# Kernel optimization log

Hardware: AMD Instinct MI355X
Metric: run time of the kernel (lower is better)

## Reference

```python
import jax, jax.numpy as jnp
import numpy as np

RANK = 3
NUM_STEPS = 3
NUM_ENT = 40000
NUM_EMB = 24
NUM_OPS = 12
DIM = 128
HID = 128
BATCH = 128
NNZ = 300000


def _lstm_dir(x, Wih, Whh, bih, bhh, reverse=False):
    # x: (S, B, D); PyTorch gate order i, f, g, o
    B = x.shape[1]
    H = Whh.shape[1]
    def step(carry, xt):
        h, c = carry
        z = xt @ Wih.T + h @ Whh.T + bih + bhh  # (B, 4H)
        i, f, g, o = jnp.split(z, 4, axis=-1)
        c = jax.nn.sigmoid(f) * c + jax.nn.sigmoid(i) * jnp.tanh(g)
        h = jax.nn.sigmoid(o) * jnp.tanh(c)
        return (h, c), h
    init = (jnp.zeros((B, H), x.dtype), jnp.zeros((B, H), x.dtype))
    _, hs = jax.lax.scan(step, init, x, reverse=reverse)
    return hs  # (S, B, H)


def _spmm(memory, src, dst, val, num_ent):
    # memory: (B, E); edges (src -> dst): out[b, j] = sum_{e: dst[e]=j} memory[b, src[e]] * val[e]
    g = memory[:, src] * val[None, :]              # (B, nnz)
    out = jax.ops.segment_sum(g.T, dst, num_segments=num_ent)  # (E, B)
    return out.T


def setup_inputs() -> dict:
    key = jax.random.key(0)
    ks = jax.random.split(key, 16)
    inp = {
        'queries': jax.random.randint(ks[0], (BATCH,), 0, NUM_EMB),
        'heads': jax.random.randint(ks[1], (BATCH,), 0, NUM_ENT),
        'edge_src': jax.random.randint(ks[2], (NUM_OPS, NNZ), 0, NUM_ENT, dtype=jnp.int32),
        'edge_dst': jax.random.randint(ks[3], (NUM_OPS, NNZ), 0, NUM_ENT, dtype=jnp.int32),
        'edge_val': jax.random.uniform(ks[4], (NUM_OPS, NNZ), jnp.float32),
        'emb': jax.random.normal(ks[5], (NUM_EMB, DIM), jnp.float32) * 0.1,
        'Wih_f': jax.random.normal(ks[6], (RANK, 4 * HID, DIM), jnp.float32) * 0.1,
        'Whh_f': jax.random.normal(ks[7], (RANK, 4 * HID, HID), jnp.float32) * 0.1,
        'bih_f': jnp.zeros((RANK, 4 * HID), jnp.float32),
        'bhh_f': jnp.zeros((RANK, 4 * HID), jnp.float32),
        'Wih_b': jax.random.normal(ks[8], (RANK, 4 * HID, DIM), jnp.float32) * 0.1,
        'Whh_b': jax.random.normal(ks[9], (RANK, 4 * HID, HID), jnp.float32) * 0.1,
        'bih_b': jnp.zeros((RANK, 4 * HID), jnp.float32),
        'bhh_b': jnp.zeros((RANK, 4 * HID), jnp.float32),
        'W0': jax.random.normal(ks[10], (2 * HID, NUM_OPS + 1), jnp.float32) * 0.1,
        'b0': jnp.zeros((1, NUM_OPS + 1), jnp.float32),
    }
    return inp


def reference(queries, heads, edge_src, edge_dst, edge_val, emb,
              Wih_f, Whh_f, bih_f, bhh_f, Wih_b, Whh_b, bih_b, bhh_b, W0, b0):
    # query embedding replicated over time: (S, B, D)
    q = emb[queries]
    x = jnp.broadcast_to(q[None], (NUM_STEPS, q.shape[0], q.shape[1]))
    head_onehot = jax.nn.one_hot(heads, NUM_ENT, dtype=jnp.float32)  # (B, E)

    logits = jnp.zeros((q.shape[0], NUM_ENT), jnp.float32)
    for r in range(RANK):
        hf = _lstm_dir(x, Wih_f[r], Whh_f[r], bih_f[r], bhh_f[r], reverse=False)
        hb = _lstm_dir(x, Wih_b[r], Whh_b[r], bih_b[r], bhh_b[r], reverse=True)
        rnn_out = jnp.concatenate([hf, hb], axis=-1)          # (S, B, 2H)
        trans = rnn_out @ W0 + b0                             # (S, B, ops+1)
        attn = jax.nn.softmax(trans, axis=-1)
        attn = jnp.transpose(attn, (0, 2, 1))                 # (S, ops+1, B)

        memory = head_onehot                                  # (B, E)
        for t in range(NUM_STEPS):
            attn_t = attn[t]                                  # (ops+1, B)
            acc = memory * attn_t[-1][:, None]                # identity operator
            for op in range(NUM_OPS):
                prod = _spmm(memory, edge_src[op], edge_dst[op], edge_val[op], NUM_ENT)
                acc = acc + prod * attn_t[op][:, None]
            memory = acc
        norm = jnp.maximum(jnp.float32(1e-20), jnp.sum(memory, axis=1, keepdims=True))
        logits = logits + memory / norm
    return logits
```

## Files before the change

kernel.cpp:

```cpp
#include <hip/hip_runtime.h>

#define NENT 40000
#define NB 128
#define NQ 24
#define NOPS 12
#define EPO 300000
#define NTOT (NOPS * EPO)
#define NRANK 3
#define NPASS 8
#define CP 16
#define ECAP 160

typedef float v4f __attribute__((ext_vector_type(4)));

__device__ __forceinline__ v4f shfl_xor4(v4f x, int m) {
    v4f r;
    r.x = __shfl_xor(x.x, m);
    r.y = __shfl_xor(x.y, m);
    r.z = __shfl_xor(x.z, m);
    r.w = __shfl_xor(x.w, m);
    return r;
}

__device__ __forceinline__ bool bittest(const unsigned* bm, int i) {
    return (bm[i >> 5] >> (i & 31)) & 1u;
}

__global__ void headmark_kernel(const int* __restrict__ heads, unsigned* __restrict__ bmH,
                                unsigned* __restrict__ bm2) {
    int h = heads[threadIdx.x];
    atomicOr(&bmH[h >> 5], 1u << (h & 31));
    atomicOr(&bm2[h >> 5], 1u << (h & 31));
}

__global__ void mark2_kernel(const int* __restrict__ src, const int* __restrict__ dst,
                             const unsigned* __restrict__ bmH, unsigned* __restrict__ bm2) {
    int i = blockIdx.x * 256 + threadIdx.x;
    if (i < NTOT) {
        int s = src[i];
        if (bittest(bmH, s)) {
            int d = dst[i];
            atomicOr(&bm2[d >> 5], 1u << (d & 31));
        }
    }
}

__global__ void build_ell_kernel(const int* __restrict__ src, const int* __restrict__ dst,
                                 const float* __restrict__ val, const unsigned* __restrict__ bm2,
                                 int* __restrict__ fillD, int* __restrict__ fillS,
                                 int2* __restrict__ eD, int2* __restrict__ eS) {
    int i = blockIdx.x * 256 + threadIdx.x;
    if (i >= NTOT) return;
    int s = src[i], d = dst[i];
    int op = i / EPO;
    int v = __float_as_int(val[i]);
    int pd = atomicAdd(&fillD[d], 1);
    eD[(size_t)d * ECAP + pd] = make_int2(s | (op << 16), v);
    if (bittest(bm2, s)) {
        int ps = atomicAdd(&fillS[s], 1);
        eS[(size_t)s * ECAP + ps] = make_int2(d | (op << 16), v);
    }
}

__global__ void zxq_kernel(const float* __restrict__ emb,
                           const float* __restrict__ Wih_f, const float* __restrict__ bih_f,
                           const float* __restrict__ bhh_f,
                           const float* __restrict__ Wih_b, const float* __restrict__ bih_b,
                           const float* __restrict__ bhh_b,
                           float* __restrict__ zxq) {
    int combo = blockIdx.x / NQ;
    int q = blockIdx.x % NQ;
    int dir = combo / 3, r = combo % 3;
    const float* Wih = (dir ? Wih_b : Wih_f) + r * 512 * 128;
    const float* bih = (dir ? bih_b : bih_f) + r * 512;
    const float* bhh = (dir ? bhh_b : bhh_f) + r * 512;
    __shared__ float x[128];
    int u = threadIdx.x;
    x[u] = emb[q * 128 + u];
    __syncthreads();
    const float* W0p = Wih + u * 128;
    const float* W1p = Wih + (128 + u) * 128;
    const float* W2p = Wih + (256 + u) * 128;
    const float* W3p = Wih + (384 + u) * 128;
    float a0 = 0.f, a1 = 0.f, a2 = 0.f, a3 = 0.f;
    for (int d = 0; d < 128; ++d) {
        float xv = x[d];
        a0 = fmaf(xv, W0p[d], a0);
        a1 = fmaf(xv, W1p[d], a1);
        a2 = fmaf(xv, W2p[d], a2);
        a3 = fmaf(xv, W3p[d], a3);
    }
    float* o = zxq + (size_t)(combo * NQ + q) * 512;
    o[u]       = a0 + bih[u]       + bhh[u];
    o[128 + u] = a1 + bih[128 + u] + bhh[128 + u];
    o[256 + u] = a2 + bih[256 + u] + bhh[256 + u];
    o[384 + u] = a3 + bih[384 + u] + bhh[384 + u];
}

__global__ void lstmq_kernel(const float* __restrict__ Whh_f, const float* __restrict__ Whh_b,
                             const float* __restrict__ zxq, float* __restrict__ hq) {
    int combo = blockIdx.x / NQ;
    int q = blockIdx.x % NQ;
    int dir = combo / 3, r = combo % 3;
    const float* Whh = (dir ? Whh_b : Whh_f) + r * 512 * 128;
    __shared__ float h[128];
    int u = threadIdx.x;
    const float* z = zxq + (size_t)(combo * NQ + q) * 512;
    float zi0 = z[u], zf0 = z[128 + u], zg0 = z[256 + u], zo0 = z[384 + u];
    const float* Wi = Whh + u * 128;
    const float* Wf = Whh + (128 + u) * 128;
    const float* Wg = Whh + (256 + u) * 128;
    const float* Wo = Whh + (384 + u) * 128;
    float c = 0.f;
    h[u] = 0.f;
    for (int s = 0; s < 3; ++s) {
        __syncthreads();
        float a0 = 0.f, a1 = 0.f, a2 = 0.f, a3 = 0.f;
        for (int d = 0; d < 128; ++d) {
            float hv = h[d];
            a0 = fmaf(hv, Wi[d], a0);
            a1 = fmaf(hv, Wf[d], a1);
            a2 = fmaf(hv, Wg[d], a2);
            a3 = fmaf(hv, Wo[d], a3);
        }
        float ig = 1.f / (1.f + expf(-(zi0 + a0)));
        float fg = 1.f / (1.f + expf(-(zf0 + a1)));
        float gg = tanhf(zg0 + a2);
        float og = 1.f / (1.f + expf(-(zo0 + a3)));
        c = fg * c + ig * gg;
        float hn = og * tanhf(c);
        __syncthreads();
        h[u] = hn;
        hq[(size_t)((combo * 3 + s) * NQ + q) * 128 + u] = hn;
    }
}

__global__ void attnq_kernel(const float* __restrict__ hq, const float* __restrict__ W0,
                             const float* __restrict__ b0, float* __restrict__ attnq) {
    int r = blockIdx.x / 3, t = blockIdx.x % 3;
    __shared__ float W0s[256 * 13];
    for (int idx = threadIdx.x; idx < 256 * 13; idx += 32) W0s[idx] = W0[idx];
    __syncthreads();
    int q = threadIdx.x;
    if (q >= NQ) return;
    float acc[13];
    for (int k = 0; k < 13; ++k) acc[k] = b0[k];
    const float* hf = hq + (size_t)(((0 * 3 + r) * 3 + t) * NQ + q) * 128;
    const float* hb = hq + (size_t)(((1 * 3 + r) * 3 + (2 - t)) * NQ + q) * 128;
    for (int u = 0; u < 128; ++u) {
        float v = hf[u];
        for (int k = 0; k < 13; ++k) acc[k] = fmaf(v, W0s[u * 13 + k], acc[k]);
    }
    for (int u = 0; u < 128; ++u) {
        float v = hb[u];
        for (int k = 0; k < 13; ++k) acc[k] = fmaf(v, W0s[(128 + u) * 13 + k], acc[k]);
    }
    float m = acc[0];
    for (int k = 1; k < 13; ++k) m = fmaxf(m, acc[k]);
    float e[13];
    float sum = 0.f;
    for (int k = 0; k < 13; ++k) { e[k] = expf(acc[k] - m); sum += e[k]; }
    float inv = 1.f / sum;
    float* ao = attnq + (size_t)(r * 3 + t) * 13 * NQ;
    for (int k = 0; k < 13; ++k) ao[k * NQ + q] = e[k] * inv;
}

__global__ void expand_kernel(const int* __restrict__ queries, const float* __restrict__ attnq,
                              float* __restrict__ attn) {
    __shared__ int qs[128];
    if (threadIdx.x < 128) qs[threadIdx.x] = queries[threadIdx.x];
    __syncthreads();
    for (int idx = threadIdx.x; idx < 9 * 13 * 128; idx += 256) {
        int b = idx & 127, kk = idx >> 7;
        attn[idx] = attnq[kk * NQ + qs[b]];
    }
}

__global__ void fused01_kernel(const int* __restrict__ heads, const float* __restrict__ attn,
                               const int* __restrict__ fillS, const int2* __restrict__ eS,
                               float* __restrict__ mem2) {
    int r = blockIdx.y;
    int b = blockIdx.x;
    int chunk = blockIdx.z;
    __shared__ float c0s[13], c1s[13];
    if (threadIdx.x < 13) {
        c0s[threadIdx.x] = attn[(size_t)((r * 3 + 0) * 13 + threadIdx.x) * 128 + b];
        c1s[threadIdx.x] = attn[(size_t)((r * 3 + 1) * 13 + threadIdx.x) * 128 + b];
    }
    __syncthreads();
    int h = heads[b];
    int lenH = fillS[h];
    float* mem = mem2 + ((size_t)(r * NPASS + (b >> 4)) * NENT) * CP + (b & 15);
    int g = threadIdx.x >> 3, lane8 = threadIdx.x & 7;
    for (int ent = g + chunk * 32; ent < lenH + 1; ent += 64) {
        int i; float wv;
        if (ent == 0) { i = h; wv = c0s[12]; }
        else {
            int2 e = eS[(size_t)h * ECAP + ent - 1];
            i = e.x & 0xFFFF;
            wv = __int_as_float(e.y) * c0s[e.x >> 16];
        }
        if (lane8 == 0) atomicAdd(&mem[(size_t)i * CP], c1s[12] * wv);
        int lenI = fillS[i];
        const int2* ei = eS + (size_t)i * ECAP;
        for (int f = lane8; f < lenI; f += 8) {
            int2 e2 = ei[f];
            atomicAdd(&mem[(size_t)(e2.x & 0xFFFF) * CP],
                      __int_as_float(e2.y) * c1s[e2.x >> 16] * wv);
        }
    }
}

struct EStage { int2 a, b, c, d; };
struct GStage { v4f a, b, c, d; };

#define ISSUE_E(E, bb) { int bi = (bb) + slot; \
    E.a = edp0[bi < l0 ? bi : 0]; \
    E.b = edp1[bi < l1 ? bi : 0]; \
    E.c = edp2[bi < l2 ? bi : 0]; \
    E.d = edp3[bi < l3 ? bi : 0]; }

#define ISSUE_G(G, E) { \
    G.a = *(const v4f*)(inr + (size_t)(E.a.x & 0xFFFF) * CP + cq4); \
    G.b = *(const v4f*)(inr + (size_t)(E.b.x & 0xFFFF) * CP + cq4); \
    G.c = *(const v4f*)(inr + (size_t)(E.c.x & 0xFFFF) * CP + cq4); \
    G.d = *(const v4f*)(inr + (size_t)(E.d.x & 0xFFFF) * CP + cq4); }

#define CONSUME_P(G, E, bb) { int bi = (bb) + slot; \
    { v4f cc = *(const v4f*)&cs[(E.a.x >> 16) * 20 + cq4]; \
      float w = bi < l0 ? __int_as_float(E.a.y) : 0.f; acc0 += (w * cc) * G.a; } \
    { v4f cc = *(const v4f*)&cs[(E.b.x >> 16) * 20 + cq4]; \
      float w = bi < l1 ? __int_as_float(E.b.y) : 0.f; acc1 += (w * cc) * G.b; } \
    { v4f cc = *(const v4f*)&cs[(E.c.x >> 16) * 20 + cq4]; \
      float w = bi < l2 ? __int_as_float(E.c.y) : 0.f; acc2 += (w * cc) * G.c; } \
    { v4f cc = *(const v4f*)&cs[(E.d.x >> 16) * 20 + cq4]; \
      float w = bi < l3 ? __int_as_float(E.d.y) : 0.f; acc3 += (w * cc) * G.d; } }

#define REDUCE_ROW(A, T) { \
    v4f red = A; \
    red += shfl_xor4(red, 4); \
    red += shfl_xor4(red, 8); \
    red += shfl_xor4(red, 16); \
    red += shfl_xor4(red, 32); \
    if (slot == 0) { \
        int j = jw + (T); \
        v4f mi = *(const v4f*)(inr + (size_t)j * CP + cq4); \
        v4f res = cid * mi + red; \
        *(v4f*)(outr + (size_t)j * CP + cq4) = res; \
        rsum += res; \
    } }

__global__ __launch_bounds__(256) void dense_kernel(const float* __restrict__ attn,
                                                    const int* __restrict__ fillD,
                                                    const int2* __restrict__ edgesD,
                                                    const float* __restrict__ in,
                                                    float* __restrict__ out,
                                                    float* __restrict__ normv) {
    int p = blockIdx.x;
    int r = blockIdx.z;
    __shared__ __align__(16) float cs[13 * 20];
    __shared__ float npart[4][16];
    int tid = threadIdx.x;
    if (tid < 13 * 16) {
        int op = tid >> 4, c0 = tid & 15;
        cs[op * 20 + c0] = attn[(size_t)((r * 3 + 2) * 13 + op) * 128 + p * CP + c0];
    }
    __syncthreads();
    int wave = tid >> 6, lane = tid & 63;
    int slot = lane >> 2;
    int cq4 = (lane & 3) * 4;
    int jw = blockIdx.y * 16 + wave * 4;
    const float* inr = in + (size_t)(r * NPASS + p) * NENT * CP;
    float* outr = out + (size_t)(r * NPASS + p) * NENT * CP;
    int l0 = fillD[jw], l1 = fillD[jw + 1], l2 = fillD[jw + 2], l3 = fillD[jw + 3];
    const int2* edp0 = edgesD + (size_t)(jw + 0) * ECAP;
    const int2* edp1 = edgesD + (size_t)(jw + 1) * ECAP;
    const int2* edp2 = edgesD + (size_t)(jw + 2) * ECAP;
    const int2* edp3 = edgesD + (size_t)(jw + 3) * ECAP;
    int maxlen = max(max(l0, l1), max(l2, l3));
    v4f acc0 = (v4f)0.f, acc1 = (v4f)0.f, acc2 = (v4f)0.f, acc3 = (v4f)0.f;

    EStage E0, E1, E2;
    GStage G0, G1, G2;
    ISSUE_E(E0, 0)
    ISSUE_E(E1, 16)
    ISSUE_E(E2, 32)
    ISSUE_G(G0, E0)
    ISSUE_G(G1, E1)
    int nb = (maxlen + 15) >> 4;
    int R = (nb + 2) / 3;
    int base = 0;
    for (int rr = 0; rr < R; ++rr, base += 48) {
        CONSUME_P(G0, E0, base)
        ISSUE_E(E0, base + 48)
        ISSUE_G(G2, E2)
        CONSUME_P(G1, E1, base + 16)
        ISSUE_E(E1, base + 64)
        ISSUE_G(G0, E0)
        CONSUME_P(G2, E2, base + 32)
        ISSUE_E(E2, base + 80)
        ISSUE_G(G1, E1)
    }

    v4f cid = *(const v4f*)&cs[12 * 20 + cq4];
    v4f rsum = (v4f)0.f;
    REDUCE_ROW(acc0, 0)
    REDUCE_ROW(acc1, 1)
    REDUCE_ROW(acc2, 2)
    REDUCE_ROW(acc3, 3)
    if (slot == 0) *(v4f*)&npart[wave][cq4] = rsum;
    __syncthreads();
    if (tid < 16) {
        float s = npart[0][tid] + npart[1][tid] + npart[2][tid] + npart[3][tid];
        atomicAdd(&normv[r * 128 + p * CP + tid], s);
    }
}

__global__ void rnorm_kernel(const float* __restrict__ normv, float* __restrict__ rnormv) {
    int i = threadIdx.x;
    rnormv[i] = 1.f / fmaxf(normv[i], 1e-20f);
}

__global__ void final_kernel(const float* __restrict__ mem3, const float* __restrict__ rnormv,
                             float* __restrict__ out) {
    __shared__ float tile[32 * 129];
    __shared__ float rn[384];
    for (int idx = threadIdx.x; idx < 384; idx += 256) rn[idx] = rnormv[idx];
    __syncthreads();
    int j0 = blockIdx.x * 32;
    for (int p = 0; p < NPASS; ++p) {
        for (int it = 0; it < 2; ++it) {
            int lin = it * 256 + threadIdx.x;
            int jj = lin >> 4, c = lin & 15;
            int b = p * CP + c;
            float s = 0.f;
            for (int r = 0; r < 3; ++r)
                s += mem3[((size_t)(r * NPASS + p) * NENT + j0 + jj) * CP + c] * rn[r * 128 + b];
            tile[jj * 129 + b] = s;
        }
    }
    __syncthreads();
    for (int it = 0; it < 16; ++it) {
        int lin = it * 256 + threadIdx.x;
        int b = lin >> 5, jj = lin & 31;
        out[(size_t)b * NENT + j0 + jj] = tile[jj * 129 + b];
    }
}

extern "C" void kernel_launch(void* const* d_in, const int* in_sizes, int n_in,
                              void* d_out, int out_size, void* d_ws, size_t ws_size,
                              hipStream_t stream) {
    const int*   queries  = (const int*)d_in[0];
    const int*   heads    = (const int*)d_in[1];
    const int*   edge_src = (const int*)d_in[2];
    const int*   edge_dst = (const int*)d_in[3];
    const float* edge_val = (const float*)d_in[4];
    const float* emb      = (const float*)d_in[5];
    const float* Wih_f    = (const float*)d_in[6];
    const float* Whh_f    = (const float*)d_in[7];
    const float* bih_f    = (const float*)d_in[8];
    const float* bhh_f    = (const float*)d_in[9];
    const float* Wih_b    = (const float*)d_in[10];
    const float* Whh_b    = (const float*)d_in[11];
    const float* bih_b    = (const float*)d_in[12];
    const float* bhh_b    = (const float*)d_in[13];
    const float* W0       = (const float*)d_in[14];
    const float* b0       = (const float*)d_in[15];
    float* out = (float*)d_out;

    char* w = (char*)d_ws;
    size_t off = 0;
    auto alloc = [&](size_t bytes) -> void* {
        off = (off + 255) & ~(size_t)255;
        void* p = w + off;
        off += bytes;
        return p;
    };
    float* attnq  = (float*)alloc((size_t)9 * 13 * NQ * sizeof(float));
    float* attn   = (float*)alloc((size_t)9 * 13 * 128 * sizeof(float));
    float* zxq    = (float*)alloc((size_t)6 * NQ * 512 * sizeof(float));
    float* hq     = (float*)alloc((size_t)6 * 3 * NQ * 128 * sizeof(float));
    unsigned* bmH = (unsigned*)alloc((2 * 1250 + 2 * NENT) * sizeof(int));
    unsigned* bm2 = bmH + 1250;
    int* fillD    = (int*)(bm2 + 1250);
    int* fillS    = fillD + NENT;
    int2*  eD     = (int2*)alloc((size_t)NENT * ECAP * sizeof(int2));
    float* mem2   = (float*)alloc((size_t)NRANK * NENT * NB * sizeof(float));
    float* mem3   = (float*)alloc((size_t)NRANK * NENT * NB * sizeof(float));
    int2*  eS     = (int2*)mem3;
    float* normv  = (float*)alloc((size_t)NRANK * NB * sizeof(float));
    float* rnormv = (float*)alloc((size_t)NRANK * NB * sizeof(float));

    int cooGrid = (NTOT + 255) / 256;

    hipMemsetAsync(bmH, 0, (2 * 1250 + 2 * NENT) * sizeof(int), stream);
    headmark_kernel<<<1, 128, 0, stream>>>(heads, bmH, bm2);
    mark2_kernel<<<cooGrid, 256, 0, stream>>>(edge_src, edge_dst, bmH, bm2);
    build_ell_kernel<<<cooGrid, 256, 0, stream>>>(edge_src, edge_dst, edge_val, bm2,
                                                  fillD, fillS, eD, eS);

    zxq_kernel<<<6 * NQ, 128, 0, stream>>>(emb, Wih_f, bih_f, bhh_f, Wih_b, bih_b, bhh_b, zxq);
    lstmq_kernel<<<6 * NQ, 128, 0, stream>>>(Whh_f, Whh_b, zxq, hq);
    attnq_kernel<<<9, 32, 0, stream>>>(hq, W0, b0, attnq);
    expand_kernel<<<1, 256, 0, stream>>>(queries, attnq, attn);

    hipMemsetAsync(mem2, 0, (size_t)NRANK * NENT * NB * sizeof(float), stream);
    hipMemsetAsync(normv, 0, NRANK * NB * sizeof(float), stream);
    {
        dim3 g(NB, NRANK, 2);
        fused01_kernel<<<g, 256, 0, stream>>>(heads, attn, fillS, eS, mem2);
    }
    {
        dim3 g(NPASS, NENT / 16, NRANK);
        dense_kernel<<<g, 256, 0, stream>>>(attn, fillD, eD, mem2, mem3, normv);
    }

    rnorm_kernel<<<1, NRANK * NB, 0, stream>>>(normv, rnormv);
    final_kernel<<<NENT / 32, 256, 0, stream>>>(mem3, rnormv, out);
}
```

Before: 1.271 ms.

## Process all three ranks per dense block to share edge loads

The dense SpMM kernel now handles all three ranks in a single block instead of one rank per grid z-slice. Each ELL edge entry is loaded once and reused for three gathers, which cuts edge-list traffic and index decoding by a factor of three. The hand-written three-stage software pipeline of edge and gather loads is replaced by a simple loop. This trades the explicit latency hiding and some occupancy (twelve accumulators, a third as many blocks) for fewer redundant edge loads.

```diff
diff --git a/kernel.cpp b/kernel.cpp
--- a/kernel.cpp
+++ b/kernel.cpp
@@ -211,32 +211,19 @@
     }
 }
 
-struct EStage { int2 a, b, c, d; };
-struct GStage { v4f a, b, c, d; };
-
-#define ISSUE_E(E, bb) { int bi = (bb) + slot; \
-    E.a = edp0[bi < l0 ? bi : 0]; \
-    E.b = edp1[bi < l1 ? bi : 0]; \
-    E.c = edp2[bi < l2 ? bi : 0]; \
-    E.d = edp3[bi < l3 ? bi : 0]; }
-
-#define ISSUE_G(G, E) { \
-    G.a = *(const v4f*)(inr + (size_t)(E.a.x & 0xFFFF) * CP + cq4); \
-    G.b = *(const v4f*)(inr + (size_t)(E.b.x & 0xFFFF) * CP + cq4); \
-    G.c = *(const v4f*)(inr + (size_t)(E.c.x & 0xFFFF) * CP + cq4); \
-    G.d = *(const v4f*)(inr + (size_t)(E.d.x & 0xFFFF) * CP + cq4); }
-
-#define CONSUME_P(G, E, bb) { int bi = (bb) + slot; \
-    { v4f cc = *(const v4f*)&cs[(E.a.x >> 16) * 20 + cq4]; \
-      float w = bi < l0 ? __int_as_float(E.a.y) : 0.f; acc0 += (w * cc) * G.a; } \
-    { v4f cc = *(const v4f*)&cs[(E.b.x >> 16) * 20 + cq4]; \
-      float w = bi < l1 ? __int_as_float(E.b.y) : 0.f; acc1 += (w * cc) * G.b; } \
-    { v4f cc = *(const v4f*)&cs[(E.c.x >> 16) * 20 + cq4]; \
-      float w = bi < l2 ? __int_as_float(E.c.y) : 0.f; acc2 += (w * cc) * G.c; } \
-    { v4f cc = *(const v4f*)&cs[(E.d.x >> 16) * 20 + cq4]; \
-      float w = bi < l3 ? __int_as_float(E.d.y) : 0.f; acc3 += (w * cc) * G.d; } }
-
-#define REDUCE_ROW(A, T) { \
+#define CSR 260
+
+#define CONSUME_ROW(E, W, T) { \
+    int row = E.x & 0xFFFF; \
+    v4f g0 = *(const v4f*)(inr0 + (size_t)row * CP + cq4); \
+    v4f g1 = *(const v4f*)(inr1 + (size_t)row * CP + cq4); \
+    v4f g2 = *(const v4f*)(inr2 + (size_t)row * CP + cq4); \
+    int cb = (E.x >> 16) * 20 + cq4; \
+    acc0##T += (W * *(const v4f*)&cs[cb]) * g0; \
+    acc1##T += (W * *(const v4f*)&cs[CSR + cb]) * g1; \
+    acc2##T += (W * *(const v4f*)&cs[2 * CSR + cb]) * g2; }
+
+#define REDUCE_ONE(A, INR, OUTR, CID, RS, T) { \
     v4f red = A; \
     red += shfl_xor4(red, 4); \
     red += shfl_xor4(red, 8); \
@@ -244,10 +231,10 @@
     red += shfl_xor4(red, 32); \
     if (slot == 0) { \
         int j = jw + (T); \
-        v4f mi = *(const v4f*)(inr + (size_t)j * CP + cq4); \
-        v4f res = cid * mi + red; \
-        *(v4f*)(outr + (size_t)j * CP + cq4) = res; \
-        rsum += res; \
+        v4f mi = *(const v4f*)(INR + (size_t)j * CP + cq4); \
+        v4f res = CID * mi + red; \
+        *(v4f*)(OUTR + (size_t)j * CP + cq4) = res; \
+        RS += res; \
     } }
 
 __global__ __launch_bounds__(256) void dense_kernel(const float* __restrict__ attn,
@@ -257,62 +244,80 @@
                                                     float* __restrict__ out,
                                                     float* __restrict__ normv) {
     int p = blockIdx.x;
-    int r = blockIdx.z;
-    __shared__ __align__(16) float cs[13 * 20];
-    __shared__ float npart[4][16];
+    __shared__ __align__(16) float cs[3 * CSR];
+    __shared__ float npart[3][4][16];
     int tid = threadIdx.x;
     if (tid < 13 * 16) {
         int op = tid >> 4, c0 = tid & 15;
-        cs[op * 20 + c0] = attn[(size_t)((r * 3 + 2) * 13 + op) * 128 + p * CP + c0];
+#pragma unroll
+        for (int r = 0; r < 3; ++r)
+            cs[r * CSR + op * 20 + c0] =
+                attn[(size_t)((r * 3 + 2) * 13 + op) * 128 + p * CP + c0];
     }
     __syncthreads();
     int wave = tid >> 6, lane = tid & 63;
     int slot = lane >> 2;
     int cq4 = (lane & 3) * 4;
     int jw = blockIdx.y * 16 + wave * 4;
-    const float* inr = in + (size_t)(r * NPASS + p) * NENT * CP;
-    float* outr = out + (size_t)(r * NPASS + p) * NENT * CP;
+    const float* inr0 = in + (size_t)(0 * NPASS + p) * NENT * CP;
+    const float* inr1 = in + (size_t)(1 * NPASS + p) * NENT * CP;
+    const float* inr2 = in + (size_t)(2 * NPASS + p) * NENT * CP;
+    float* outr0 = out + (size_t)(0 * NPASS + p) * NENT * CP;
+    float* outr1 = out + (size_t)(1 * NPASS + p) * NENT * CP;
+    float* outr2 = out + (size_t)(2 * NPASS + p) * NENT * CP;
     int l0 = fillD[jw], l1 = fillD[jw + 1], l2 = fillD[jw + 2], l3 = fillD[jw + 3];
     const int2* edp0 = edgesD + (size_t)(jw + 0) * ECAP;
     const int2* edp1 = edgesD + (size_t)(jw + 1) * ECAP;
     const int2* edp2 = edgesD + (size_t)(jw + 2) * ECAP;
     const int2* edp3 = edgesD + (size_t)(jw + 3) * ECAP;
     int maxlen = max(max(l0, l1), max(l2, l3));
-    v4f acc0 = (v4f)0.f, acc1 = (v4f)0.f, acc2 = (v4f)0.f, acc3 = (v4f)0.f;
-
-    EStage E0, E1, E2;
-    GStage G0, G1, G2;
-    ISSUE_E(E0, 0)
-    ISSUE_E(E1, 16)
-    ISSUE_E(E2, 32)
-    ISSUE_G(G0, E0)
-    ISSUE_G(G1, E1)
-    int nb = (maxlen + 15) >> 4;
-    int R = (nb + 2) / 3;
-    int base = 0;
-    for (int rr = 0; rr < R; ++rr, base += 48) {
-        CONSUME_P(G0, E0, base)
-        ISSUE_E(E0, base + 48)
-        ISSUE_G(G2, E2)
-        CONSUME_P(G1, E1, base + 16)
-        ISSUE_E(E1, base + 64)
-        ISSUE_G(G0, E0)
-        CONSUME_P(G2, E2, base + 32)
-        ISSUE_E(E2, base + 80)
-        ISSUE_G(G1, E1)
-    }
-
-    v4f cid = *(const v4f*)&cs[12 * 20 + cq4];
-    v4f rsum = (v4f)0.f;
-    REDUCE_ROW(acc0, 0)
-    REDUCE_ROW(acc1, 1)
-    REDUCE_ROW(acc2, 2)
-    REDUCE_ROW(acc3, 3)
-    if (slot == 0) *(v4f*)&npart[wave][cq4] = rsum;
-    __syncthreads();
-    if (tid < 16) {
-        float s = npart[0][tid] + npart[1][tid] + npart[2][tid] + npart[3][tid];
-        atomicAdd(&normv[r * 128 + p * CP + tid], s);
+
+    v4f acc00 = (v4f)0.f, acc01 = (v4f)0.f, acc02 = (v4f)0.f, acc03 = (v4f)0.f;
+    v4f acc10 = (v4f)0.f, acc11 = (v4f)0.f, acc12 = (v4f)0.f, acc13 = (v4f)0.f;
+    v4f acc20 = (v4f)0.f, acc21 = (v4f)0.f, acc22 = (v4f)0.f, acc23 = (v4f)0.f;
+
+    for (int base = 0; base < maxlen; base += 16) {
+        int bi = base + slot;
+        int2 e0 = edp0[bi < l0 ? bi : 0];
+        int2 e1 = edp1[bi < l1 ? bi : 0];
+        int2 e2 = edp2[bi < l2 ? bi : 0];
+        int2 e3 = edp3[bi < l3 ? bi : 0];
+        float w0 = bi < l0 ? __int_as_float(e0.y) : 0.f;
+        float w1 = bi < l1 ? __int_as_float(e1.y) : 0.f;
+        float w2 = bi < l2 ? __int_as_float(e2.y) : 0.f;
+        float w3 = bi < l3 ? __int_as_float(e3.y) : 0.f;
+        CONSUME_ROW(e0, w0, 0)
+        CONSUME_ROW(e1, w1, 1)
+        CONSUME_ROW(e2, w2, 2)
+        CONSUME_ROW(e3, w3, 3)
+    }
+
+    v4f cid0 = *(const v4f*)&cs[12 * 20 + cq4];
+    v4f cid1 = *(const v4f*)&cs[CSR + 12 * 20 + cq4];
+    v4f cid2 = *(const v4f*)&cs[2 * CSR + 12 * 20 + cq4];
+    v4f rs0 = (v4f)0.f, rs1 = (v4f)0.f, rs2 = (v4f)0.f;
+    REDUCE_ONE(acc00, inr0, outr0, cid0, rs0, 0)
+    REDUCE_ONE(acc01, inr0, outr0, cid0, rs0, 1)
+    REDUCE_ONE(acc02, inr0, outr0, cid0, rs0, 2)
+    REDUCE_ONE(acc03, inr0, outr0, cid0, rs0, 3)
+    REDUCE_ONE(acc10, inr1, outr1, cid1, rs1, 0)
+    REDUCE_ONE(acc11, inr1, outr1, cid1, rs1, 1)
+    REDUCE_ONE(acc12, inr1, outr1, cid1, rs1, 2)
+    REDUCE_ONE(acc13, inr1, outr1, cid1, rs1, 3)
+    REDUCE_ONE(acc20, inr2, outr2, cid2, rs2, 0)
+    REDUCE_ONE(acc21, inr2, outr2, cid2, rs2, 1)
+    REDUCE_ONE(acc22, inr2, outr2, cid2, rs2, 2)
+    REDUCE_ONE(acc23, inr2, outr2, cid2, rs2, 3)
+    if (slot == 0) {
+        *(v4f*)&npart[0][wave][cq4] = rs0;
+        *(v4f*)&npart[1][wave][cq4] = rs1;
+        *(v4f*)&npart[2][wave][cq4] = rs2;
+    }
+    __syncthreads();
+    if (tid < 48) {
+        int r = tid >> 4, c = tid & 15;
+        float s = npart[r][0][c] + npart[r][1][c] + npart[r][2][c] + npart[r][3][c];
+        atomicAdd(&normv[r * 128 + p * CP + c], s);
     }
 }
 
@@ -411,7 +416,7 @@
         fused01_kernel<<<g, 256, 0, stream>>>(heads, attn, fillS, eS, mem2);
     }
     {
-        dim3 g(NPASS, NENT / 16, NRANK);
+        dim3 g(NPASS, NENT / 16);
         dense_kernel<<<g, 256, 0, stream>>>(attn, fillD, eD, mem2, mem3, normv);
     }
 
```

After: 1.433 ms. 1.13x slower.
